# Kernel tuning notes

Hardware: AMD Instinct MI355X
Metric: run time of the kernel (lower is better)

## Reference

```python
import jax, jax.numpy as jnp
import numpy as np

N_NODES = 50000
N_EDGES = 800000
F_IN = 256
HEADS = 8
OUT_CH = 10  # hard-coded in the source GATv2Conv(in, 10, heads=H)
HIDDEN = HEADS * OUT_CH  # 80
NEG_SLOPE = 0.2  # PyG GATv2Conv default


def _gatv2_layer(x, src, dst, Wl, Wr, att, b, n):
    """One GATv2Conv layer (eval mode, concat=True, self-loops already added).
    x: [n, F_in]; src/dst: [E_tot] int; Wl/Wr: [F_in, H*C]; att: [H, C]; b: [H*C].
    """
    xl = (x @ Wl).reshape(n, HEADS, OUT_CH)  # source-side transform
    xr = (x @ Wr).reshape(n, HEADS, OUT_CH)  # target-side transform
    # gather -> LeakyReLU -> attention logit per edge/head
    e = jax.nn.leaky_relu(xl[src] + xr[dst], NEG_SLOPE)      # [E, H, C]
    logits = jnp.einsum('ehc,hc->eh', e, att)                # [E, H]
    # segment softmax over incoming edges of each target node
    m = jax.ops.segment_max(logits, dst, num_segments=n)     # [n, H]
    ex = jnp.exp(logits - m[dst])
    denom = jax.ops.segment_sum(ex, dst, num_segments=n)     # [n, H]
    alpha = ex / (denom[dst] + 1e-16)                        # [E, H]
    # scatter-add aggregation of weighted source messages
    out = jax.ops.segment_sum(xl[src] * alpha[:, :, None], dst, num_segments=n)
    return out.reshape(n, HIDDEN) + b


def _gat_forward(x, edge_index, params):
    n = x.shape[0]
    loops = jnp.arange(n, dtype=edge_index.dtype)
    src = jnp.concatenate([edge_index[0], loops])  # add self loops (PyG default)
    dst = jnp.concatenate([edge_index[1], loops])
    for (Wl, Wr, att, b) in params:
        x = jax.nn.elu(_gatv2_layer(x, src, dst, Wl, Wr, att, b, n))
    return x


def setup_inputs() -> dict:
    key = jax.random.key(0)
    ks = jax.random.split(key, 16)
    x = jax.random.normal(ks[0], (N_NODES, F_IN), dtype=jnp.float32)
    edge_index = jax.random.randint(ks[1], (2, N_EDGES), 0, N_NODES, dtype=jnp.int64)
    inp = {'x': x, 'edge_index': edge_index}
    dims_in = [F_IN, HIDDEN, HIDDEN]
    for i, d_in in enumerate(dims_in):
        k0, k1, k2 = jax.random.split(ks[2 + i], 3)
        s = 1.0 / np.sqrt(d_in)
        inp[f'Wl{i}'] = jax.random.normal(k0, (d_in, HIDDEN), dtype=jnp.float32) * s
        inp[f'Wr{i}'] = jax.random.normal(k1, (d_in, HIDDEN), dtype=jnp.float32) * s
        inp[f'att{i}'] = jax.random.normal(k2, (HEADS, OUT_CH), dtype=jnp.float32) * 0.1
        inp[f'b{i}'] = jnp.zeros((HIDDEN,), dtype=jnp.float32)
    return inp


def reference(x, edge_index, Wl0, Wr0, att0, b0, Wl1, Wr1, att1, b1, Wl2, Wr2, att2, b2):
    params = [(Wl0, Wr0, att0, b0), (Wl1, Wr1, att1, b1), (Wl2, Wr2, att2, b2)]
    return _gat_forward(x, edge_index, params)
```

## Files before the change

### kernel.cpp

```cpp
#include <hip/hip_runtime.h>
#include <math.h>

#define N_NODES 50000
#define N_EDGES 800000
#define E_TOT   (N_EDGES + N_NODES)
#define HEADS   8
#define OUTC    10
#define HID     80
#define NEG_SLOPE 0.2f


__global__ __launch_bounds__(256) void hist_k(const int* __restrict__ ei, int* __restrict__ cnt) {
    int e = blockIdx.x * blockDim.x + threadIdx.x;
    if (e >= E_TOT) return;
    int d = (e < N_EDGES) ? ei[N_EDGES + e] : (e - N_EDGES);
    atomicAdd(&cnt[d], 1);
}

__global__ __launch_bounds__(1024) void scan_k(const int* __restrict__ cnt, int* __restrict__ rowptr) {
    __shared__ int wsum[16];
    __shared__ int carry_s;
    const int tid = threadIdx.x;
    const int lane = tid & 63, wid = tid >> 6;
    if (tid == 0) carry_s = 0;
    __syncthreads();
    for (int base = 0; base < N_NODES; base += 1024) {
        int i = base + tid;
        int v = (i < N_NODES) ? cnt[i] : 0;
        int s = v;
        #pragma unroll
        for (int off = 1; off < 64; off <<= 1) {
            int t = __shfl_up(s, off, 64);
            if (lane >= off) s += t;
        }
        if (lane == 63) wsum[wid] = s;
        int carry = carry_s;
        __syncthreads();
        if (wid == 0 && lane < 16) {
            int w = wsum[lane];
            #pragma unroll
            for (int off = 1; off < 16; off <<= 1) {
                int t = __shfl_up(w, off, 16);
                if (lane >= off) w += t;
            }
            wsum[lane] = w;
        }
        __syncthreads();
        int woff = (wid > 0) ? wsum[wid - 1] : 0;
        int incl = s + woff;
        int excl = incl - v;
        if (i < N_NODES) rowptr[i] = carry + excl;
        int total = wsum[15];
        __syncthreads();
        if (tid == 0) carry_s = carry + total;
        __syncthreads();
    }
    if (tid == 0) rowptr[N_NODES] = carry_s;
}

__global__ __launch_bounds__(256) void scatter_k(const int* __restrict__ ei,
                                                 const int* __restrict__ rowptr,
                                                 int* __restrict__ cursor,
                                                 int* __restrict__ csr) {
    int e = blockIdx.x * blockDim.x + threadIdx.x;
    if (e >= E_TOT) return;
    int s, d;
    if (e < N_EDGES) { s = ei[e]; d = ei[N_EDGES + e]; }
    else { s = e - N_EDGES; d = s; }
    int pos = rowptr[d] + atomicAdd(&cursor[d], 1);
    csr[pos] = s;
}


#define TC 20
__global__ __launch_bounds__(256) void gemm2_k(const float* __restrict__ A, int K,
                                               const float* __restrict__ Wl,
                                               const float* __restrict__ Wr,
                                               float* __restrict__ xl,
                                               float* __restrict__ xr) {
    const int lane = threadIdx.x & 63;
    const int wv = __builtin_amdgcn_readfirstlane(threadIdx.x >> 6);
    const int rg = blockIdx.x >> 1;
    const int cb = blockIdx.x & 1;
    const int row = rg * 64 + lane;
    const int j0 = wv * TC;

    const float* __restrict__ W = cb ? Wr : Wl;
    float* __restrict__ Xo = cb ? xr : xl;

    const int r = (row < N_NODES) ? row : (N_NODES - 1);
    const float* __restrict__ Ar = A + (size_t)r * K;

    float acc[TC];
    #pragma unroll
    for (int j = 0; j < TC; ++j) acc[j] = 0.f;

    for (int kb = 0; kb < K; kb += 4) {
        const float4 a = *reinterpret_cast<const float4*>(Ar + kb);
        #pragma unroll
        for (int t = 0; t < 4; ++t) {
            const float av = (t == 0) ? a.x : (t == 1) ? a.y : (t == 2) ? a.z : a.w;
            const float* __restrict__ wrow = W + (size_t)(kb + t) * HID + j0;
            #pragma unroll
            for (int q = 0; q < 5; ++q) {
                const float4 w = *reinterpret_cast<const float4*>(wrow + q * 4);
                acc[q * 4 + 0] = fmaf(av, w.x, acc[q * 4 + 0]);
                acc[q * 4 + 1] = fmaf(av, w.y, acc[q * 4 + 1]);
                acc[q * 4 + 2] = fmaf(av, w.z, acc[q * 4 + 2]);
                acc[q * 4 + 3] = fmaf(av, w.w, acc[q * 4 + 3]);
            }
        }
    }

    if (row < N_NODES) {
        float* op = Xo + (size_t)row * HID + j0;
        #pragma unroll
        for (int q = 0; q < 5; ++q)
            *reinterpret_cast<float4*>(op + q * 4) =
                make_float4(acc[q * 4 + 0], acc[q * 4 + 1], acc[q * 4 + 2], acc[q * 4 + 3]);
    }
}


__global__ __launch_bounds__(256) void agg_k(const float* __restrict__ xl,
                                             const float* __restrict__ xr,
                                             const int* __restrict__ rowptr,
                                             const int* __restrict__ csr,
                                             const float* __restrict__ att,
                                             const float* __restrict__ bias,
                                             float* __restrict__ out) {
    const int tid = threadIdx.x;
    const int lane = tid & 63;
    const int node = blockIdx.x * 4 + (tid >> 6);
    if (node >= N_NODES) return;
    const int g = lane >> 4;
    const int u = lane & 15;
    const int cb = u * 5;

    float att5[5], xr5[5];
    #pragma unroll
    for (int c = 0; c < 5; ++c) {
        att5[c] = att[cb + c];
        xr5[c] = xr[(size_t)node * HID + cb + c];
    }
    const int ro = rowptr[node];
    const int deg = rowptr[node + 1] - ro;

    float m = -INFINITY, s = 0.f;
    float acc[5] = {0.f, 0.f, 0.f, 0.f, 0.f};

    for (int i = g; i < deg; i += 4) {
        const int src = csr[ro + i];
        const float* xlp = xl + (size_t)src * HID + cb;
        float xl5[5];
        float part = 0.f;
        #pragma unroll
        for (int c = 0; c < 5; ++c) {
            xl5[c] = xlp[c];
            float e = xl5[c] + xr5[c];
            e = (e > 0.f) ? e : NEG_SLOPE * e;
            part = fmaf(e, att5[c], part);
        }
        const float logit = part + __shfl_xor(part, 1, 64);
        const float nm = fmaxf(m, logit);
        const float scale = __expf(m - nm);
        const float p = __expf(logit - nm);
        s = s * scale + p;
        #pragma unroll
        for (int c = 0; c < 5; ++c) acc[c] = acc[c] * scale + p * xl5[c];
        m = nm;
    }

    #pragma unroll
    for (int off = 16; off <= 32; off <<= 1) {
        const float om = __shfl_xor(m, off, 64);
        const float os = __shfl_xor(s, off, 64);
        float oacc[5];
        #pragma unroll
        for (int c = 0; c < 5; ++c) oacc[c] = __shfl_xor(acc[c], off, 64);
        const float nm = fmaxf(m, om);
        const float sc1 = (m == -INFINITY) ? 0.f : __expf(m - nm);
        const float sc2 = (om == -INFINITY) ? 0.f : __expf(om - nm);
        s = s * sc1 + os * sc2;
        #pragma unroll
        for (int c = 0; c < 5; ++c) acc[c] = acc[c] * sc1 + oacc[c] * sc2;
        m = nm;
    }

    if (g == 0) {
        const float inv = 1.f / (s + 1e-16f);
        #pragma unroll
        for (int c = 0; c < 5; ++c) {
            float v = acc[c] * inv + bias[cb + c];
            v = (v > 0.f) ? v : (__expf(v) - 1.f);
            out[(size_t)node * HID + cb + c] = v;
        }
    }
}


extern "C" void kernel_launch(void* const* d_in, const int* in_sizes, int n_in,
                              void* d_out, int out_size, void* d_ws, size_t ws_size,
                              hipStream_t stream) {
    const float* x  = (const float*)d_in[0];
    const int*   ei = (const int*)d_in[1];
    const float* Wl[3]   = {(const float*)d_in[2], (const float*)d_in[6],  (const float*)d_in[10]};
    const float* Wr[3]   = {(const float*)d_in[3], (const float*)d_in[7],  (const float*)d_in[11]};
    const float* attp[3] = {(const float*)d_in[4], (const float*)d_in[8],  (const float*)d_in[12]};
    const float* bp[3]   = {(const float*)d_in[5], (const float*)d_in[9],  (const float*)d_in[13]};

    char* ws = (char*)d_ws;
    size_t off = 0;
    auto alloc = [&](size_t bytes) -> void* {
        void* p = ws + off;
        off += (bytes + 255) & ~(size_t)255;
        return p;
    };
    int* cnt    = (int*)alloc((size_t)N_NODES * 4);
    int* cursor = (int*)alloc((size_t)N_NODES * 4);
    int* rowptr = (int*)alloc((size_t)(N_NODES + 1) * 4);
    int* csr    = (int*)alloc((size_t)E_TOT * 4);
    float* xl   = (float*)alloc((size_t)N_NODES * HID * 4);
    float* xr   = (float*)alloc((size_t)N_NODES * HID * 4);
    float* actA = (float*)alloc((size_t)N_NODES * HID * 4);
    float* actB = (float*)alloc((size_t)N_NODES * HID * 4);

    hipMemsetAsync(cnt, 0, (size_t)N_NODES * 4, stream);
    hipMemsetAsync(cursor, 0, (size_t)N_NODES * 4, stream);

    hist_k<<<(E_TOT + 255) / 256, 256, 0, stream>>>(ei, cnt);
    scan_k<<<1, 1024, 0, stream>>>(cnt, rowptr);
    scatter_k<<<(E_TOT + 255) / 256, 256, 0, stream>>>(ei, rowptr, cursor, csr);

    for (int l = 0; l < 3; ++l) {
        const float* act_in = (l == 0) ? x : (l == 1 ? actA : actB);
        const int K = (l == 0) ? 256 : 80;
        gemm2_k<<<1564, 256, 0, stream>>>(act_in, K, Wl[l], Wr[l], xl, xr);
        float* out_l = (l == 0) ? actA : (l == 1 ? actB : (float*)d_out);
        agg_k<<<N_NODES / 4, 256, 0, stream>>>(xl, xr, rowptr, csr, attp[l], bp[l], out_l);
    }
}
```

Measured before the change: 506.2 us.

## Share A tile via LDS across Wl/Wr GEMM and remap aggregation to per-head lanes

The projection GEMM now computes both xl and xr for 64 rows in one block. It stages 16-wide chunks of the input rows in shared memory so A is read from global memory once instead of twice, and each wave computes 40 output columns. The aggregation kernel assigns one lane per head with all 10 channels. This removes the cross-lane shuffle for the logit and processes 8 edges in parallel per wave instead of 4, giving more memory-level parallelism on the gathers. The cost is more register pressure (40 and 10-wide accumulators), extra barriers in the GEMM, and non-vectorized 10-float gathers.

```diff
diff --git a/kernel.cpp b/kernel.cpp
--- a/kernel.cpp
+++ b/kernel.cpp
@@ -72,125 +72,140 @@
 }
 
 
-#define TC 20
-__global__ __launch_bounds__(256) void gemm2_k(const float* __restrict__ A, int K,
+__global__ __launch_bounds__(256) void gemm3_k(const float* __restrict__ A, int K,
                                                const float* __restrict__ Wl,
                                                const float* __restrict__ Wr,
                                                float* __restrict__ xl,
                                                float* __restrict__ xr) {
-    const int lane = threadIdx.x & 63;
-    const int wv = __builtin_amdgcn_readfirstlane(threadIdx.x >> 6);
-    const int rg = blockIdx.x >> 1;
-    const int cb = blockIdx.x & 1;
-    const int row = rg * 64 + lane;
-    const int j0 = wv * TC;
-
-    const float* __restrict__ W = cb ? Wr : Wl;
-    float* __restrict__ Xo = cb ? xr : xl;
-
-    const int r = (row < N_NODES) ? row : (N_NODES - 1);
-    const float* __restrict__ Ar = A + (size_t)r * K;
-
-    float acc[TC];
-    #pragma unroll
-    for (int j = 0; j < TC; ++j) acc[j] = 0.f;
-
-    for (int kb = 0; kb < K; kb += 4) {
-        const float4 a = *reinterpret_cast<const float4*>(Ar + kb);
-        #pragma unroll
-        for (int t = 0; t < 4; ++t) {
-            const float av = (t == 0) ? a.x : (t == 1) ? a.y : (t == 2) ? a.z : a.w;
-            const float* __restrict__ wrow = W + (size_t)(kb + t) * HID + j0;
+    __shared__ float4 sa[64][4];
+    const int tid = threadIdx.x;
+    const int lane = tid & 63;
+    const int wv = __builtin_amdgcn_readfirstlane(tid >> 6);
+    const int mat = wv >> 1;
+    const int j0 = (wv & 1) * 40;
+    const int row0 = blockIdx.x * 64;
+    const int row = row0 + lane;
+
+    const float* __restrict__ W = mat ? Wr : Wl;
+    float* __restrict__ Xo = mat ? xr : xl;
+
+    const int lr = tid >> 2;
+    const int lq = tid & 3;
+    const int lrow = (row0 + lr < N_NODES) ? (row0 + lr) : (N_NODES - 1);
+    const float* __restrict__ Asrc = A + (size_t)lrow * K + lq * 4;
+
+    float acc[40];
+    #pragma unroll
+    for (int j = 0; j < 40; ++j) acc[j] = 0.f;
+
+    for (int kb = 0; kb < K; kb += 16) {
+        sa[lr][lq] = *reinterpret_cast<const float4*>(Asrc + kb);
+        __syncthreads();
+
+        float4 ar[4];
+        #pragma unroll
+        for (int q = 0; q < 4; ++q) ar[q] = sa[lane][q];
+
+        #pragma unroll
+        for (int q = 0; q < 4; ++q) {
             #pragma unroll
-            for (int q = 0; q < 5; ++q) {
-                const float4 w = *reinterpret_cast<const float4*>(wrow + q * 4);
-                acc[q * 4 + 0] = fmaf(av, w.x, acc[q * 4 + 0]);
-                acc[q * 4 + 1] = fmaf(av, w.y, acc[q * 4 + 1]);
-                acc[q * 4 + 2] = fmaf(av, w.z, acc[q * 4 + 2]);
-                acc[q * 4 + 3] = fmaf(av, w.w, acc[q * 4 + 3]);
+            for (int t = 0; t < 4; ++t) {
+                const float av = (t == 0) ? ar[q].x : (t == 1) ? ar[q].y
+                               : (t == 2) ? ar[q].z : ar[q].w;
+                const float* __restrict__ wrow = W + (size_t)(kb + q * 4 + t) * HID + j0;
+                #pragma unroll
+                for (int c4 = 0; c4 < 10; ++c4) {
+                    const float4 w = *reinterpret_cast<const float4*>(wrow + c4 * 4);
+                    acc[c4 * 4 + 0] = fmaf(av, w.x, acc[c4 * 4 + 0]);
+                    acc[c4 * 4 + 1] = fmaf(av, w.y, acc[c4 * 4 + 1]);
+                    acc[c4 * 4 + 2] = fmaf(av, w.z, acc[c4 * 4 + 2]);
+                    acc[c4 * 4 + 3] = fmaf(av, w.w, acc[c4 * 4 + 3]);
+                }
             }
         }
+        __syncthreads();
     }
 
     if (row < N_NODES) {
         float* op = Xo + (size_t)row * HID + j0;
         #pragma unroll
-        for (int q = 0; q < 5; ++q)
-            *reinterpret_cast<float4*>(op + q * 4) =
-                make_float4(acc[q * 4 + 0], acc[q * 4 + 1], acc[q * 4 + 2], acc[q * 4 + 3]);
-    }
-}
-
-
-__global__ __launch_bounds__(256) void agg_k(const float* __restrict__ xl,
-                                             const float* __restrict__ xr,
-                                             const int* __restrict__ rowptr,
-                                             const int* __restrict__ csr,
-                                             const float* __restrict__ att,
-                                             const float* __restrict__ bias,
-                                             float* __restrict__ out) {
+        for (int c4 = 0; c4 < 10; ++c4)
+            *reinterpret_cast<float4*>(op + c4 * 4) =
+                make_float4(acc[c4 * 4 + 0], acc[c4 * 4 + 1], acc[c4 * 4 + 2], acc[c4 * 4 + 3]);
+    }
+}
+
+
+__global__ __launch_bounds__(256) void agg2_k(const float* __restrict__ xl,
+                                              const float* __restrict__ xr,
+                                              const int* __restrict__ rowptr,
+                                              const int* __restrict__ csr,
+                                              const float* __restrict__ att,
+                                              const float* __restrict__ bias,
+                                              float* __restrict__ out) {
     const int tid = threadIdx.x;
     const int lane = tid & 63;
     const int node = blockIdx.x * 4 + (tid >> 6);
     if (node >= N_NODES) return;
-    const int g = lane >> 4;
-    const int u = lane & 15;
-    const int cb = u * 5;
-
-    float att5[5], xr5[5];
-    #pragma unroll
-    for (int c = 0; c < 5; ++c) {
-        att5[c] = att[cb + c];
-        xr5[c] = xr[(size_t)node * HID + cb + c];
+    const int eg = lane >> 3;
+    const int h = lane & 7;
+    const int cb = h * 10;
+
+    float att10[10], xr10[10];
+    #pragma unroll
+    for (int c = 0; c < 10; ++c) {
+        att10[c] = att[cb + c];
+        xr10[c] = xr[(size_t)node * HID + cb + c];
     }
     const int ro = rowptr[node];
     const int deg = rowptr[node + 1] - ro;
 
     float m = -INFINITY, s = 0.f;
-    float acc[5] = {0.f, 0.f, 0.f, 0.f, 0.f};
-
-    for (int i = g; i < deg; i += 4) {
+    float acc[10];
+    #pragma unroll
+    for (int c = 0; c < 10; ++c) acc[c] = 0.f;
+
+    for (int i = eg; i < deg; i += 8) {
         const int src = csr[ro + i];
         const float* xlp = xl + (size_t)src * HID + cb;
-        float xl5[5];
-        float part = 0.f;
-        #pragma unroll
-        for (int c = 0; c < 5; ++c) {
-            xl5[c] = xlp[c];
-            float e = xl5[c] + xr5[c];
+        float xl10[10];
+        float logit = 0.f;
+        #pragma unroll
+        for (int c = 0; c < 10; ++c) {
+            xl10[c] = xlp[c];
+            float e = xl10[c] + xr10[c];
             e = (e > 0.f) ? e : NEG_SLOPE * e;
-            part = fmaf(e, att5[c], part);
-        }
-        const float logit = part + __shfl_xor(part, 1, 64);
+            logit = fmaf(e, att10[c], logit);
+        }
         const float nm = fmaxf(m, logit);
         const float scale = __expf(m - nm);
         const float p = __expf(logit - nm);
         s = s * scale + p;
         #pragma unroll
-        for (int c = 0; c < 5; ++c) acc[c] = acc[c] * scale + p * xl5[c];
+        for (int c = 0; c < 10; ++c) acc[c] = acc[c] * scale + p * xl10[c];
         m = nm;
     }
 
     #pragma unroll
-    for (int off = 16; off <= 32; off <<= 1) {
+    for (int off = 8; off <= 32; off <<= 1) {
         const float om = __shfl_xor(m, off, 64);
         const float os = __shfl_xor(s, off, 64);
-        float oacc[5];
-        #pragma unroll
-        for (int c = 0; c < 5; ++c) oacc[c] = __shfl_xor(acc[c], off, 64);
+        float oacc[10];
+        #pragma unroll
+        for (int c = 0; c < 10; ++c) oacc[c] = __shfl_xor(acc[c], off, 64);
         const float nm = fmaxf(m, om);
         const float sc1 = (m == -INFINITY) ? 0.f : __expf(m - nm);
         const float sc2 = (om == -INFINITY) ? 0.f : __expf(om - nm);
         s = s * sc1 + os * sc2;
         #pragma unroll
-        for (int c = 0; c < 5; ++c) acc[c] = acc[c] * sc1 + oacc[c] * sc2;
+        for (int c = 0; c < 10; ++c) acc[c] = acc[c] * sc1 + oacc[c] * sc2;
         m = nm;
     }
 
-    if (g == 0) {
+    if (lane < 8) {
         const float inv = 1.f / (s + 1e-16f);
         #pragma unroll
-        for (int c = 0; c < 5; ++c) {
+        for (int c = 0; c < 10; ++c) {
             float v = acc[c] * inv + bias[cb + c];
             v = (v > 0.f) ? v : (__expf(v) - 1.f);
             out[(size_t)node * HID + cb + c] = v;
@@ -235,8 +250,8 @@
     for (int l = 0; l < 3; ++l) {
         const float* act_in = (l == 0) ? x : (l == 1 ? actA : actB);
         const int K = (l == 0) ? 256 : 80;
-        gemm2_k<<<1564, 256, 0, stream>>>(act_in, K, Wl[l], Wr[l], xl, xr);
+        gemm3_k<<<(N_NODES + 63) / 64, 256, 0, stream>>>(act_in, K, Wl[l], Wr[l], xl, xr);
         float* out_l = (l == 0) ? actA : (l == 1 ? actB : (float*)d_out);
-        agg_k<<<N_NODES / 4, 256, 0, stream>>>(xl, xr, rowptr, csr, attp[l], bp[l], out_l);
-    }
-}
+        agg2_k<<<N_NODES / 4, 256, 0, stream>>>(xl, xr, rowptr, csr, attp[l], bp[l], out_l);
+    }
+}
```

After: 557.2 us. +10.1%, slower.
